# Kernel optimization log

Measured on AMD Instinct MI355X. Metric: run time of the kernel, lower is better.

## Reference

```python
import jax, jax.numpy as jnp
import numpy as np

N_DST = 25000
LEAKY = 0.2
EPS = 1e-5


def _params(dim_node=128, dim_edge=128, dim_time=100, dim_out=128):
    ks = jax.random.split(jax.random.key(1), 8)
    dq = dim_node + dim_time
    dk = dim_node + dim_edge + dim_time
    do = dim_node + dim_out
    p = {
        'w_t': jnp.asarray((1.0 / 10 ** np.linspace(0, 9, dim_time, dtype=np.float32)).reshape(dim_time, 1)),
        'b_t': jnp.zeros((dim_time,), jnp.float32),
        'Wq': jax.random.normal(ks[0], (dim_out, dq), jnp.float32) * (dq ** -0.5),
        'bq': jnp.zeros((dim_out,), jnp.float32),
        'Wk': jax.random.normal(ks[1], (dim_out, dk), jnp.float32) * (dk ** -0.5),
        'bk': jnp.zeros((dim_out,), jnp.float32),
        'Wv': jax.random.normal(ks[2], (dim_out, dk), jnp.float32) * (dk ** -0.5),
        'bv': jnp.zeros((dim_out,), jnp.float32),
        'Wout': jax.random.normal(ks[3], (dim_out, do), jnp.float32) * (do ** -0.5),
        'bout': jnp.zeros((dim_out,), jnp.float32),
        'ln_w': jnp.ones((dim_out,), jnp.float32),
        'ln_b': jnp.zeros((dim_out,), jnp.float32),
    }
    return p


def setup_inputs() -> dict:
    key = jax.random.key(0)
    k1, k2, k3, k4, k5 = jax.random.split(key, 5)
    E = 400000
    inp = {
        'h': jax.random.normal(k1, (425000, 128), jnp.float32),
        'f': jax.random.normal(k2, (E, 128), jnp.float32),
        'dt': jax.random.uniform(k3, (E,), jnp.float32) * 1e4,
        'src_idx': jax.random.randint(k4, (E,), 0, 425000, jnp.int32),
        'dst_idx': jax.random.randint(k5, (E,), 0, N_DST, jnp.int32),
    }
    inp.update(_params())
    return inp


def reference(h, f, dt, src_idx, dst_idx, w_t, b_t, Wq, bq, Wk, bk, Wv, bv, Wout, bout, ln_w, ln_b):
    num_head = 2
    dim_out = Wq.shape[0]
    E = dt.shape[0]
    # time encoding: cos(Linear(t))
    time_feat = jnp.cos(dt[:, None] * w_t[:, 0][None, :] + b_t)        # [E, dt]
    zero_time = jnp.cos(b_t)[None, :]                                   # [1, dt]
    zero_time_feat = jnp.broadcast_to(zero_time, (N_DST, b_t.shape[0]))
    # Q from dst nodes (first N_DST rows of h), gathered per edge
    q_nodes = jnp.concatenate([h[:N_DST], zero_time_feat], axis=1) @ Wq.T + bq  # [N_DST, dim_out]
    Q = q_nodes[dst_idx]                                                # [E, dim_out]
    kv_in = jnp.concatenate([h[src_idx], f, time_feat], axis=1)         # [E, dn+de+dt]
    K = kv_in @ Wk.T + bk
    V = kv_in @ Wv.T + bv
    dh = dim_out // num_head
    Qh = Q.reshape(E, num_head, dh)
    Kh = K.reshape(E, num_head, dh)
    Vh = V.reshape(E, num_head, dh)
    score = jax.nn.leaky_relu(jnp.sum(Qh * Kh, axis=2), LEAKY)          # [E, H]
    # edge softmax over incoming edges per dst node
    m = jax.ops.segment_max(score, dst_idx, num_segments=N_DST)         # [N_DST, H]
    e = jnp.exp(score - m[dst_idx])
    s = jax.ops.segment_sum(e, dst_idx, num_segments=N_DST)
    att = e / s[dst_idx]                                                # [E, H]
    Vw = (Vh * att[:, :, None]).reshape(E, dim_out)
    agg = jax.ops.segment_sum(Vw, dst_idx, num_segments=N_DST)          # [N_DST, dim_out]
    rst = jnp.concatenate([agg, h[:N_DST]], axis=1) @ Wout.T + bout
    rst = jax.nn.relu(rst)
    mu = jnp.mean(rst, axis=-1, keepdims=True)
    var = jnp.mean((rst - mu) ** 2, axis=-1, keepdims=True)
    return (rst - mu) * jax.lax.rsqrt(var + EPS) * ln_w + ln_b
```

## Files before the change

### kernel.cpp

```cpp
#include <hip/hip_runtime.h>
#include <math.h>

#define N_DST   25000
#define DN      128
#define DE      128
#define DTF     100
#define DKV     356
#define KP      384
#define DQ      228
#define DOUT    128
#define LEAKY   0.2f
#define LN_EPS  1e-5f
#define LDA     392

#define OFF_V       0ull
#define OFF_SCORE   102400000ull
#define OFF_QN      105600000ull
#define OFF_WS      118400000ull
#define OFF_WT      118700000ull
#define OFF_CNT     118900000ull
#define OFF_OFFS    119000000ull
#define OFF_CURSOR  119100004ull
#define OFF_RANK    119200004ull

typedef __attribute__((ext_vector_type(8))) short short8;
typedef __attribute__((ext_vector_type(4))) float f32x4;

__device__ __forceinline__ unsigned short f2bf(float x) {
    union { float f; unsigned u; } v; v.f = x;
    unsigned r = v.u + 0x7FFFu + ((v.u >> 16) & 1u);
    return (unsigned short)(r >> 16);
}
__device__ __forceinline__ float bf2f(unsigned short u) {
    union { unsigned u; float f; } v; v.u = ((unsigned)u) << 16;
    return v.f;
}

__global__ __launch_bounds__(128) void k_prepw(const float* __restrict__ Wk,
                                               const float* __restrict__ Wv,
                                               unsigned short* __restrict__ WS) {
    const int n = blockIdx.x;
    const float* src = (n < 128) ? &Wk[(size_t)n * DKV] : &Wv[(size_t)(n - 128) * DKV];
    const int c16 = n >> 4, t16 = n & 15;
    for (int k = threadIdx.x; k < KP; k += 128) {
        float v = (k < DKV) ? src[k] : 0.f;
        int kc = k >> 5, qd = (k >> 3) & 3, j = k & 7;
        WS[(size_t)(((kc * 16 + c16) * 64 + qd * 16 + t16) * 8 + j)] = f2bf(v);
    }
}

__global__ __launch_bounds__(128) void k_prepwt(const float* __restrict__ Wout,
                                                float* __restrict__ WT) {
    const int k = blockIdx.x;
    const int j = threadIdx.x;
    WT[k * 128 + j] = Wout[(size_t)j * 256 + k];
}

__global__ __launch_bounds__(128) void k_qnodes(const float* __restrict__ h,
                                                const float* __restrict__ Wq,
                                                const float* __restrict__ bq,
                                                const float* __restrict__ b_t,
                                                float* __restrict__ qn) {
    __shared__ float wq_s[128 * 132];
    __shared__ float hrow[8 * 128];
    const int j = threadIdx.x;

    for (int k4 = 0; k4 < 128; k4 += 4) {
        float4 w = *(const float4*)&Wq[j * DQ + k4];
        *(float4*)&wq_s[j * 132 + k4] = w;
    }
    float cq = bq[j];
    for (int k = 0; k < DTF; ++k)
        cq += Wq[j * DQ + 128 + k] * cosf(b_t[k]);
    __syncthreads();

    for (int r0 = blockIdx.x * 8; r0 < N_DST; r0 += gridDim.x * 8) {
        for (int u = j; u < 256; u += 128) {
            int rr = u >> 5, q = u & 31;
            int r = r0 + rr;
            float4 v = make_float4(0.f, 0.f, 0.f, 0.f);
            if (r < N_DST) v = *(const float4*)&h[(size_t)r * DN + q * 4];
            *(float4*)&hrow[rr * 128 + q * 4] = v;
        }
        __syncthreads();
        float acc[8];
        #pragma unroll
        for (int rr = 0; rr < 8; ++rr) acc[rr] = cq;
        for (int k4 = 0; k4 < 128; k4 += 4) {
            float4 wv = *(float4*)&wq_s[j * 132 + k4];
            #pragma unroll
            for (int rr = 0; rr < 8; ++rr) {
                float4 hv = *(float4*)&hrow[rr * 128 + k4];
                acc[rr] += hv.x * wv.x + hv.y * wv.y + hv.z * wv.z + hv.w * wv.w;
            }
        }
        #pragma unroll
        for (int rr = 0; rr < 8; ++rr)
            if (r0 + rr < N_DST) qn[(size_t)(r0 + rr) * DOUT + j] = acc[rr];
        __syncthreads();
    }
}

__global__ void k_hist(const int* __restrict__ dst, int* __restrict__ cnt, int E) {
    int i = blockIdx.x * 256 + threadIdx.x;
    if (i < E) atomicAdd(&cnt[dst[i]], 1);
}

__global__ __launch_bounds__(256) void k_scan(const int* __restrict__ cnt,
                                              int* __restrict__ offs,
                                              int* __restrict__ cursor) {
    __shared__ int totals[256];
    __shared__ int bases[257];
    const int t = threadIdx.x;
    const int STRIP = (N_DST + 255) / 256;
    int s = 0;
    for (int i = 0; i < STRIP; ++i) {
        int idx = t * STRIP + i;
        if (idx < N_DST) s += cnt[idx];
    }
    totals[t] = s;
    __syncthreads();
    if (t == 0) {
        int run = 0;
        for (int i = 0; i < 256; ++i) { bases[i] = run; run += totals[i]; }
        bases[256] = run;
    }
    __syncthreads();
    int run = bases[t];
    for (int i = 0; i < STRIP; ++i) {
        int idx = t * STRIP + i;
        if (idx < N_DST) {
            offs[idx] = run;
            cursor[idx] = run;
            run += cnt[idx];
        }
    }
    if (t == 0) offs[N_DST] = bases[256];
}

__global__ void k_scatter(const int* __restrict__ dst, int* __restrict__ cursor,
                          int* __restrict__ rank, int E) {
    int i = blockIdx.x * 256 + threadIdx.x;
    if (i < E) {
        int d = dst[i];
        int pos = atomicAdd(&cursor[d], 1);
        rank[i] = pos;
    }
}

__global__ __launch_bounds__(256, 3) void k_edge(const float* __restrict__ h,
                                                 const float* __restrict__ f,
                                                 const float* __restrict__ dtv,
                                                 const int* __restrict__ src_idx,
                                                 const int* __restrict__ dst_idx,
                                                 const int* __restrict__ rank,
                                                 const float* __restrict__ w_t,
                                                 const float* __restrict__ b_t,
                                                 const unsigned short* __restrict__ WS,
                                                 const float* __restrict__ bk,
                                                 const float* __restrict__ bv,
                                                 const float* __restrict__ qn,
                                                 unsigned short* __restrict__ Vout,
                                                 float* __restrict__ score,
                                                 int E) {
    __shared__ unsigned short At[64 * LDA];
    __shared__ int sidx[64];
    __shared__ int didx[64];
    __shared__ int rks[64];

    const int tid = threadIdx.x;
    const int e0  = blockIdx.x * 64;

    if (tid < 64) {
        int ge = min(e0 + tid, E - 1);
        sidx[tid] = src_idx[ge];
        didx[tid] = dst_idx[ge];
        rks[tid]  = rank[ge];
    }
    __syncthreads();

    {
        const int e  = tid >> 2;
        const int qb = tid & 3;
        const int ge = min(e0 + e, E - 1);
        const int s  = sidx[e];
        const float dte = dtv[ge];
        const float* hb = &h[(size_t)s * DN];
        const float* fb = &f[(size_t)ge * DE];
        float4 buf[8];

        #pragma unroll
        for (int it = 0; it < 8; ++it) buf[it] = *(const float4*)&hb[qb * 4 + it * 16];
        #pragma unroll
        for (int it = 0; it < 8; ++it) {
            int c = qb * 4 + it * 16;
            union { unsigned short us[4]; uint2 u2; } pk;
            pk.us[0] = f2bf(buf[it].x); pk.us[1] = f2bf(buf[it].y);
            pk.us[2] = f2bf(buf[it].z); pk.us[3] = f2bf(buf[it].w);
            *(uint2*)&At[e * LDA + c] = pk.u2;
        }
        #pragma unroll
        for (int it = 0; it < 8; ++it) buf[it] = *(const float4*)&fb[qb * 4 + it * 16];
        #pragma unroll
        for (int it = 0; it < 8; ++it) {
            int c = 128 + qb * 4 + it * 16;
            union { unsigned short us[4]; uint2 u2; } pk;
            pk.us[0] = f2bf(buf[it].x); pk.us[1] = f2bf(buf[it].y);
            pk.us[2] = f2bf(buf[it].z); pk.us[3] = f2bf(buf[it].w);
            *(uint2*)&At[e * LDA + c] = pk.u2;
        }
        #pragma unroll
        for (int it = 0; it < 8; ++it) {
            int t0 = qb * 4 + it * 16;
            float4 v = make_float4(0.f, 0.f, 0.f, 0.f);
            if (t0 < DTF) {
                v.x = cosf(dte * w_t[t0 + 0] + b_t[t0 + 0]);
                v.y = cosf(dte * w_t[t0 + 1] + b_t[t0 + 1]);
                v.z = cosf(dte * w_t[t0 + 2] + b_t[t0 + 2]);
                v.w = cosf(dte * w_t[t0 + 3] + b_t[t0 + 3]);
            }
            union { unsigned short us[4]; uint2 u2; } pk;
            pk.us[0] = f2bf(v.x); pk.us[1] = f2bf(v.y);
            pk.us[2] = f2bf(v.z); pk.us[3] = f2bf(v.w);
            *(uint2*)&At[e * LDA + 256 + t0] = pk.u2;
        }
    }
    __syncthreads();

    const int lane = tid & 63;
    const int w    = tid >> 6;
    const int t16  = lane & 15;
    const int qd   = lane >> 4;
    const int w4   = w * 4;

    f32x4 acc[4][4];
    #pragma unroll
    for (int r = 0; r < 4; ++r)
        #pragma unroll
        for (int c = 0; c < 4; ++c)
            acc[r][c] = (f32x4){0.f, 0.f, 0.f, 0.f};

    short8 aC[4], aN[4], bC[4], bN[4];
    #pragma unroll
    for (int r = 0; r < 4; ++r)
        aC[r] = *(const short8*)&At[(r * 16 + t16) * LDA + qd * 8];
    #pragma unroll
    for (int c = 0; c < 4; ++c)
        bC[c] = *(const short8*)(WS + (size_t)((0 * 16 + w4 + c) * 64 + lane) * 8);

    #pragma unroll 1
    for (int kc = 0; kc < 12; kc += 2) {
        #pragma unroll
        for (int r = 0; r < 4; ++r)
            aN[r] = *(const short8*)&At[(r * 16 + t16) * LDA + (kc + 1) * 32 + qd * 8];
        #pragma unroll
        for (int c = 0; c < 4; ++c)
            bN[c] = *(const short8*)(WS + (size_t)(((kc + 1) * 16 + w4 + c) * 64 + lane) * 8);
        #pragma unroll
        for (int r = 0; r < 4; ++r)
            #pragma unroll
            for (int c = 0; c < 4; ++c)
                acc[r][c] = __builtin_amdgcn_mfma_f32_16x16x32_bf16(aC[r], bC[c], acc[r][c], 0, 0, 0);
        if (kc + 2 < 12) {
            #pragma unroll
            for (int r = 0; r < 4; ++r)
                aC[r] = *(const short8*)&At[(r * 16 + t16) * LDA + (kc + 2) * 32 + qd * 8];
            #pragma unroll
            for (int c = 0; c < 4; ++c)
                bC[c] = *(const short8*)(WS + (size_t)(((kc + 2) * 16 + w4 + c) * 64 + lane) * 8);
        }
        #pragma unroll
        for (int r = 0; r < 4; ++r)
            #pragma unroll
            for (int c = 0; c < 4; ++c)
                acc[r][c] = __builtin_amdgcn_mfma_f32_16x16x32_bf16(aN[r], bN[c], acc[r][c], 0, 0, 0);
    }

    if (w >= 2) {
        const int vc0 = (w - 2) * 64;
        #pragma unroll
        for (int c = 0; c < 4; ++c) {
            const int vcol = vc0 + c * 16 + t16;
            const float bvv = bv[vcol];
            #pragma unroll
            for (int r = 0; r < 4; ++r) {
                #pragma unroll
                for (int i = 0; i < 4; ++i) {
                    int el = r * 16 + qd * 4 + i;
                    int ge = e0 + el;
                    if (ge < E)
                        Vout[(size_t)rks[el] * DOUT + vcol] = f2bf(acc[r][c][i] + bvv);
                }
            }
        }
    } else {
        float bkc[4];
        #pragma unroll
        for (int c = 0; c < 4; ++c)
            bkc[c] = bk[w * 64 + c * 16 + t16];
        #pragma unroll
        for (int r = 0; r < 4; ++r) {
            #pragma unroll
            for (int i = 0; i < 4; ++i) {
                const int el = r * 16 + qd * 4 + i;
                const int d  = didx[el];
                const float* qrow = &qn[(size_t)d * DOUT + w * 64 + t16];
                float p = (acc[r][0][i] + bkc[0]) * qrow[0]
                        + (acc[r][1][i] + bkc[1]) * qrow[16]
                        + (acc[r][2][i] + bkc[2]) * qrow[32]
                        + (acc[r][3][i] + bkc[3]) * qrow[48];
                p += __shfl_xor(p, 1);
                p += __shfl_xor(p, 2);
                p += __shfl_xor(p, 4);
                p += __shfl_xor(p, 8);
                if (t16 == 0) {
                    int ge = e0 + el;
                    if (ge < E) {
                        float sc = (p >= 0.f) ? p : LEAKY * p;
                        score[(size_t)rks[el] * 2 + w] = sc;
                    }
                }
            }
        }
    }
}

__global__ __launch_bounds__(512) void k_dst(const unsigned short* __restrict__ V,
                                             const float* __restrict__ score,
                                             const int* __restrict__ offs,
                                             const float* __restrict__ h,
                                             const float* __restrict__ WT,
                                             const float* __restrict__ bout,
                                             const float* __restrict__ ln_w,
                                             const float* __restrict__ ln_b,
                                             float* __restrict__ out) {
    const int tid = threadIdx.x;
    const int s   = tid >> 5;
    const int t32 = tid & 31;
    const int d   = blockIdx.x * 16 + s;
    const bool valid = d < N_DST;
    const int beg = valid ? offs[d] : 0;
    const int end = valid ? offs[d + 1] : 0;

    __shared__ float inc[16][256];
    __shared__ float wchunk[64 * 128];

    float m0 = -1e30f, m1 = -1e30f;
    for (int i = beg + t32; i < end; i += 32) {
        float2 sc = *(const float2*)&score[(size_t)i * 2];
        m0 = fmaxf(m0, sc.x);
        m1 = fmaxf(m1, sc.y);
    }
    #pragma unroll
    for (int o = 1; o < 32; o <<= 1) {
        m0 = fmaxf(m0, __shfl_xor(m0, o));
        m1 = fmaxf(m1, __shfl_xor(m1, o));
    }
    const int   hd = t32 >> 4;
    const float mh = hd ? m1 : m0;

    float a0 = 0.f, a1 = 0.f, a2 = 0.f, a3 = 0.f, l = 0.f;
    int i = beg;
    for (; i + 1 < end; i += 2) {
        float s0 = score[(size_t)i * 2 + hd];
        float s1 = score[(size_t)(i + 1) * 2 + hd];
        ushort4 v0 = *(const ushort4*)&V[(size_t)i * DOUT + t32 * 4];
        ushort4 v1 = *(const ushort4*)&V[(size_t)(i + 1) * DOUT + t32 * 4];
        float w0 = __expf(s0 - mh);
        float w1 = __expf(s1 - mh);
        l += w0 + w1;
        a0 += w0 * bf2f(v0.x) + w1 * bf2f(v1.x);
        a1 += w0 * bf2f(v0.y) + w1 * bf2f(v1.y);
        a2 += w0 * bf2f(v0.z) + w1 * bf2f(v1.z);
        a3 += w0 * bf2f(v0.w) + w1 * bf2f(v1.w);
    }
    if (i < end) {
        float s0 = score[(size_t)i * 2 + hd];
        ushort4 v0 = *(const ushort4*)&V[(size_t)i * DOUT + t32 * 4];
        float w0 = __expf(s0 - mh);
        l += w0;
        a0 += w0 * bf2f(v0.x);
        a1 += w0 * bf2f(v0.y);
        a2 += w0 * bf2f(v0.z);
        a3 += w0 * bf2f(v0.w);
    }
    float inv = (l > 0.f) ? (1.f / l) : 0.f;
    inc[s][t32 * 4 + 0] = a0 * inv;
    inc[s][t32 * 4 + 1] = a1 * inv;
    inc[s][t32 * 4 + 2] = a2 * inv;
    inc[s][t32 * 4 + 3] = a3 * inv;
    {
        float4 hh = make_float4(0.f, 0.f, 0.f, 0.f);
        if (valid) hh = *(const float4*)&h[(size_t)d * DN + t32 * 4];
        *(float4*)&inc[s][128 + t32 * 4] = hh;
    }

    float4 r4 = *(const float4*)&bout[t32 * 4];
    #pragma unroll 1
    for (int ch = 0; ch < 4; ++ch) {
        __syncthreads();
        for (int u = tid; u < 2048; u += 512)
            *(float4*)&wchunk[u * 4] = *(const float4*)&WT[(size_t)ch * 8192 + u * 4];
        __syncthreads();
        #pragma unroll 4
        for (int kk = 0; kk < 64; ++kk) {
            float ic = inc[s][ch * 64 + kk];
            float4 w4 = *(float4*)&wchunk[kk * 128 + t32 * 4];
            r4.x += w4.x * ic;
            r4.y += w4.y * ic;
            r4.z += w4.z * ic;
            r4.w += w4.w * ic;
        }
    }
    r4.x = fmaxf(r4.x, 0.f);
    r4.y = fmaxf(r4.y, 0.f);
    r4.z = fmaxf(r4.z, 0.f);
    r4.w = fmaxf(r4.w, 0.f);

    float s1 = r4.x + r4.y + r4.z + r4.w;
    float s2 = r4.x * r4.x + r4.y * r4.y + r4.z * r4.z + r4.w * r4.w;
    #pragma unroll
    for (int o = 1; o < 32; o <<= 1) {
        s1 += __shfl_xor(s1, o);
        s2 += __shfl_xor(s2, o);
    }
    float mu  = s1 * (1.f / 128.f);
    float var = s2 * (1.f / 128.f) - mu * mu;
    float rsd = rsqrtf(var + LN_EPS);
    if (valid) {
        float4 lw = *(const float4*)&ln_w[t32 * 4];
        float4 lb = *(const float4*)&ln_b[t32 * 4];
        float4 o4;
        o4.x = (r4.x - mu) * rsd * lw.x + lb.x;
        o4.y = (r4.y - mu) * rsd * lw.y + lb.y;
        o4.z = (r4.z - mu) * rsd * lw.z + lb.z;
        o4.w = (r4.w - mu) * rsd * lw.w + lb.w;
        *(float4*)&out[(size_t)d * DOUT + t32 * 4] = o4;
    }
}

extern "C" void kernel_launch(void* const* d_in, const int* in_sizes, int n_in,
                              void* d_out, int out_size, void* d_ws, size_t ws_size,
                              hipStream_t stream) {
    const float* h       = (const float*)d_in[0];
    const float* f       = (const float*)d_in[1];
    const float* dt      = (const float*)d_in[2];
    const int*   src_idx = (const int*)d_in[3];
    const int*   dst_idx = (const int*)d_in[4];
    const float* w_t     = (const float*)d_in[5];
    const float* b_t     = (const float*)d_in[6];
    const float* Wq      = (const float*)d_in[7];
    const float* bq      = (const float*)d_in[8];
    const float* Wk      = (const float*)d_in[9];
    const float* bk      = (const float*)d_in[10];
    const float* Wv      = (const float*)d_in[11];
    const float* bv      = (const float*)d_in[12];
    const float* Wout    = (const float*)d_in[13];
    const float* bout    = (const float*)d_in[14];
    const float* ln_w    = (const float*)d_in[15];
    const float* ln_b    = (const float*)d_in[16];
    float*       out     = (float*)d_out;

    const int E = in_sizes[2];

    char* ws = (char*)d_ws;
    unsigned short* V  = (unsigned short*)(ws + OFF_V);
    float* score       = (float*)(ws + OFF_SCORE);
    float* qn          = (float*)(ws + OFF_QN);
    unsigned short* WS = (unsigned short*)(ws + OFF_WS);
    float* WT          = (float*)(ws + OFF_WT);
    int*   cnt         = (int*)(ws + OFF_CNT);
    int*   offs        = (int*)(ws + OFF_OFFS);
    int*   cursor      = (int*)(ws + OFF_CURSOR);
    int*   rank        = (int*)(ws + OFF_RANK);

    hipMemsetAsync(cnt, 0, N_DST * sizeof(int), stream);

    k_prepw<<<256, 128, 0, stream>>>(Wk, Wv, WS);
    k_prepwt<<<256, 128, 0, stream>>>(Wout, WT);
    k_qnodes<<<512, 128, 0, stream>>>(h, Wq, bq, b_t, qn);
    k_hist<<<(E + 255) / 256, 256, 0, stream>>>(dst_idx, cnt, E);
    k_scan<<<1, 256, 0, stream>>>(cnt, offs, cursor);
    k_scatter<<<(E + 255) / 256, 256, 0, stream>>>(dst_idx, cursor, rank, E);
    k_edge<<<(E + 63) / 64, 256, 0, stream>>>(h, f, dt, src_idx, dst_idx, rank,
                                              w_t, b_t, WS, bk, bv, qn, V, score, E);
    k_dst<<<(N_DST + 15) / 16, 512, 0, stream>>>(V, score, offs, h, WT, bout,
                                                 ln_w, ln_b, out);
}
```

Measured before the change: 875.3 us.

## Write V/score in edge order, gather via CSR edge list; fast cos; rework qnodes

The edge kernel now writes V and score rows in original edge order, giving coalesced stores. k_scatter builds a CSR edge list, and the destination kernel gathers rows through that indirection instead of reading a pre-sorted layout. Time-encoding cos is replaced by a hardware cos with range reduction via fract. The Q-node projection now keeps weights in registers and splits K across two half-blocks, one block per 16 rows. Gathers in k_dst become random row reads, and the fast cos is less accurate for large arguments.

```diff
diff --git a/kernel.cpp b/kernel.cpp
--- a/kernel.cpp
+++ b/kernel.cpp
@@ -12,6 +12,7 @@
 #define LEAKY   0.2f
 #define LN_EPS  1e-5f
 #define LDA     392
+#define INV2PI  0.15915494309189535f
 
 #define OFF_V       0ull
 #define OFF_SCORE   102400000ull
@@ -21,7 +22,7 @@
 #define OFF_CNT     118900000ull
 #define OFF_OFFS    119000000ull
 #define OFF_CURSOR  119100004ull
-#define OFF_RANK    119200004ull
+#define OFF_ELIST   119200004ull
 
 typedef __attribute__((ext_vector_type(8))) short short8;
 typedef __attribute__((ext_vector_type(4))) float f32x4;
@@ -34,6 +35,9 @@
 __device__ __forceinline__ float bf2f(unsigned short u) {
     union { unsigned u; float f; } v; v.u = ((unsigned)u) << 16;
     return v.f;
+}
+__device__ __forceinline__ float fastcos(float x) {
+    return __builtin_amdgcn_cosf(__builtin_amdgcn_fractf(x * INV2PI));
 }
 
 __global__ __launch_bounds__(128) void k_prepw(const float* __restrict__ Wk,
@@ -56,48 +60,64 @@
     WT[k * 128 + j] = Wout[(size_t)j * 256 + k];
 }
 
-__global__ __launch_bounds__(128) void k_qnodes(const float* __restrict__ h,
+__global__ __launch_bounds__(256) void k_qnodes(const float* __restrict__ h,
                                                 const float* __restrict__ Wq,
                                                 const float* __restrict__ bq,
                                                 const float* __restrict__ b_t,
                                                 float* __restrict__ qn) {
-    __shared__ float wq_s[128 * 132];
-    __shared__ float hrow[8 * 128];
-    const int j = threadIdx.x;
-
-    for (int k4 = 0; k4 < 128; k4 += 4) {
-        float4 w = *(const float4*)&Wq[j * DQ + k4];
-        *(float4*)&wq_s[j * 132 + k4] = w;
-    }
-    float cq = bq[j];
-    for (int k = 0; k < DTF; ++k)
-        cq += Wq[j * DQ + 128 + k] * cosf(b_t[k]);
+    __shared__ float hrows[16 * 128];
+    __shared__ float part[16 * 128];
+    const int tid = threadIdx.x;
+    const int j  = tid & 127;
+    const int kh = tid >> 7;
+
+    float wq[64];
+    #pragma unroll
+    for (int k = 0; k < 64; k += 4) {
+        float4 w = *(const float4*)&Wq[j * DQ + kh * 64 + k];
+        wq[k] = w.x; wq[k + 1] = w.y; wq[k + 2] = w.z; wq[k + 3] = w.w;
+    }
+    float cq = 0.f;
+    if (kh == 0) {
+        cq = bq[j];
+        for (int k = 0; k < DTF; ++k)
+            cq += Wq[j * DQ + 128 + k] * fastcos(b_t[k]);
+    }
+
+    const int r0 = blockIdx.x * 16;
+    for (int u = tid; u < 512; u += 256) {
+        int rr = u >> 5, q = u & 31;
+        int r = r0 + rr;
+        float4 v = make_float4(0.f, 0.f, 0.f, 0.f);
+        if (r < N_DST) v = *(const float4*)&h[(size_t)r * DN + q * 4];
+        *(float4*)&hrows[rr * 128 + q * 4] = v;
+    }
     __syncthreads();
 
-    for (int r0 = blockIdx.x * 8; r0 < N_DST; r0 += gridDim.x * 8) {
-        for (int u = j; u < 256; u += 128) {
-            int rr = u >> 5, q = u & 31;
+    float acc[16];
+    #pragma unroll
+    for (int rr = 0; rr < 16; ++rr) acc[rr] = 0.f;
+    #pragma unroll
+    for (int k4 = 0; k4 < 64; k4 += 4) {
+        float w0 = wq[k4], w1 = wq[k4 + 1], w2 = wq[k4 + 2], w3 = wq[k4 + 3];
+        #pragma unroll
+        for (int rr = 0; rr < 16; ++rr) {
+            float4 hv = *(float4*)&hrows[rr * 128 + kh * 64 + k4];
+            acc[rr] += w0 * hv.x + w1 * hv.y + w2 * hv.z + w3 * hv.w;
+        }
+    }
+    if (kh == 1) {
+        #pragma unroll
+        for (int rr = 0; rr < 16; ++rr) part[rr * 128 + j] = acc[rr];
+    }
+    __syncthreads();
+    if (kh == 0) {
+        #pragma unroll
+        for (int rr = 0; rr < 16; ++rr) {
             int r = r0 + rr;
-            float4 v = make_float4(0.f, 0.f, 0.f, 0.f);
-            if (r < N_DST) v = *(const float4*)&h[(size_t)r * DN + q * 4];
-            *(float4*)&hrow[rr * 128 + q * 4] = v;
-        }
-        __syncthreads();
-        float acc[8];
-        #pragma unroll
-        for (int rr = 0; rr < 8; ++rr) acc[rr] = cq;
-        for (int k4 = 0; k4 < 128; k4 += 4) {
-            float4 wv = *(float4*)&wq_s[j * 132 + k4];
-            #pragma unroll
-            for (int rr = 0; rr < 8; ++rr) {
-                float4 hv = *(float4*)&hrow[rr * 128 + k4];
-                acc[rr] += hv.x * wv.x + hv.y * wv.y + hv.z * wv.z + hv.w * wv.w;
-            }
-        }
-        #pragma unroll
-        for (int rr = 0; rr < 8; ++rr)
-            if (r0 + rr < N_DST) qn[(size_t)(r0 + rr) * DOUT + j] = acc[rr];
-        __syncthreads();
+            if (r < N_DST)
+                qn[(size_t)r * DOUT + j] = acc[rr] + part[rr * 128 + j] + cq;
+        }
     }
 }
 
@@ -139,12 +159,12 @@
 }
 
 __global__ void k_scatter(const int* __restrict__ dst, int* __restrict__ cursor,
-                          int* __restrict__ rank, int E) {
+                          int* __restrict__ elist, int E) {
     int i = blockIdx.x * 256 + threadIdx.x;
     if (i < E) {
         int d = dst[i];
         int pos = atomicAdd(&cursor[d], 1);
-        rank[i] = pos;
+        elist[pos] = i;
     }
 }
 
@@ -153,7 +173,6 @@
                                                  const float* __restrict__ dtv,
                                                  const int* __restrict__ src_idx,
                                                  const int* __restrict__ dst_idx,
-                                                 const int* __restrict__ rank,
                                                  const float* __restrict__ w_t,
                                                  const float* __restrict__ b_t,
                                                  const unsigned short* __restrict__ WS,
@@ -166,7 +185,6 @@
     __shared__ unsigned short At[64 * LDA];
     __shared__ int sidx[64];
     __shared__ int didx[64];
-    __shared__ int rks[64];
 
     const int tid = threadIdx.x;
     const int e0  = blockIdx.x * 64;
@@ -175,7 +193,6 @@
         int ge = min(e0 + tid, E - 1);
         sidx[tid] = src_idx[ge];
         didx[tid] = dst_idx[ge];
-        rks[tid]  = rank[ge];
     }
     __syncthreads();
 
@@ -187,37 +204,29 @@
         const float dte = dtv[ge];
         const float* hb = &h[(size_t)s * DN];
         const float* fb = &f[(size_t)ge * DE];
-        float4 buf[8];
-
-        #pragma unroll
-        for (int it = 0; it < 8; ++it) buf[it] = *(const float4*)&hb[qb * 4 + it * 16];
-        #pragma unroll
-        for (int it = 0; it < 8; ++it) {
-            int c = qb * 4 + it * 16;
+        float4 buf[16];
+
+        #pragma unroll
+        for (int it = 0; it < 8; ++it) buf[it]     = *(const float4*)&hb[qb * 4 + it * 16];
+        #pragma unroll
+        for (int it = 0; it < 8; ++it) buf[8 + it] = *(const float4*)&fb[qb * 4 + it * 16];
+        #pragma unroll
+        for (int it = 0; it < 16; ++it) {
+            int c = (it < 8) ? (qb * 4 + it * 16) : (128 + qb * 4 + (it - 8) * 16);
             union { unsigned short us[4]; uint2 u2; } pk;
             pk.us[0] = f2bf(buf[it].x); pk.us[1] = f2bf(buf[it].y);
             pk.us[2] = f2bf(buf[it].z); pk.us[3] = f2bf(buf[it].w);
             *(uint2*)&At[e * LDA + c] = pk.u2;
         }
         #pragma unroll
-        for (int it = 0; it < 8; ++it) buf[it] = *(const float4*)&fb[qb * 4 + it * 16];
-        #pragma unroll
-        for (int it = 0; it < 8; ++it) {
-            int c = 128 + qb * 4 + it * 16;
-            union { unsigned short us[4]; uint2 u2; } pk;
-            pk.us[0] = f2bf(buf[it].x); pk.us[1] = f2bf(buf[it].y);
-            pk.us[2] = f2bf(buf[it].z); pk.us[3] = f2bf(buf[it].w);
-            *(uint2*)&At[e * LDA + c] = pk.u2;
-        }
-        #pragma unroll
         for (int it = 0; it < 8; ++it) {
             int t0 = qb * 4 + it * 16;
             float4 v = make_float4(0.f, 0.f, 0.f, 0.f);
             if (t0 < DTF) {
-                v.x = cosf(dte * w_t[t0 + 0] + b_t[t0 + 0]);
-                v.y = cosf(dte * w_t[t0 + 1] + b_t[t0 + 1]);
-                v.z = cosf(dte * w_t[t0 + 2] + b_t[t0 + 2]);
-                v.w = cosf(dte * w_t[t0 + 3] + b_t[t0 + 3]);
+                v.x = fastcos(dte * w_t[t0 + 0] + b_t[t0 + 0]);
+                v.y = fastcos(dte * w_t[t0 + 1] + b_t[t0 + 1]);
+                v.z = fastcos(dte * w_t[t0 + 2] + b_t[t0 + 2]);
+                v.w = fastcos(dte * w_t[t0 + 3] + b_t[t0 + 3]);
             }
             union { unsigned short us[4]; uint2 u2; } pk;
             pk.us[0] = f2bf(v.x); pk.us[1] = f2bf(v.y);
@@ -246,7 +255,7 @@
         aC[r] = *(const short8*)&At[(r * 16 + t16) * LDA + qd * 8];
     #pragma unroll
     for (int c = 0; c < 4; ++c)
-        bC[c] = *(const short8*)(WS + (size_t)((0 * 16 + w4 + c) * 64 + lane) * 8);
+        bC[c] = *(const short8*)(WS + (size_t)((w4 + c) * 64 + lane) * 8);
 
     #pragma unroll 1
     for (int kc = 0; kc < 12; kc += 2) {
@@ -278,18 +287,20 @@
 
     if (w >= 2) {
         const int vc0 = (w - 2) * 64;
-        #pragma unroll
-        for (int c = 0; c < 4; ++c) {
-            const int vcol = vc0 + c * 16 + t16;
-            const float bvv = bv[vcol];
+        float bvv[4];
+        #pragma unroll
+        for (int c = 0; c < 4; ++c) bvv[c] = bv[vc0 + c * 16 + t16];
+        #pragma unroll
+        for (int r = 0; r < 4; ++r) {
             #pragma unroll
-            for (int r = 0; r < 4; ++r) {
-                #pragma unroll
-                for (int i = 0; i < 4; ++i) {
-                    int el = r * 16 + qd * 4 + i;
-                    int ge = e0 + el;
-                    if (ge < E)
-                        Vout[(size_t)rks[el] * DOUT + vcol] = f2bf(acc[r][c][i] + bvv);
+            for (int i = 0; i < 4; ++i) {
+                int el = r * 16 + qd * 4 + i;
+                int ge = e0 + el;
+                if (ge < E) {
+                    unsigned short* vr = &Vout[(size_t)ge * DOUT + vc0 + t16];
+                    #pragma unroll
+                    for (int c = 0; c < 4; ++c)
+                        vr[c * 16] = f2bf(acc[r][c][i] + bvv[c]);
                 }
             }
         }
@@ -317,7 +328,7 @@
                     int ge = e0 + el;
                     if (ge < E) {
                         float sc = (p >= 0.f) ? p : LEAKY * p;
-                        score[(size_t)rks[el] * 2 + w] = sc;
+                        score[(size_t)ge * 2 + w] = sc;
                     }
                 }
             }
@@ -328,6 +339,7 @@
 __global__ __launch_bounds__(512) void k_dst(const unsigned short* __restrict__ V,
                                              const float* __restrict__ score,
                                              const int* __restrict__ offs,
+                                             const int* __restrict__ elist,
                                              const float* __restrict__ h,
                                              const float* __restrict__ WT,
                                              const float* __restrict__ bout,
@@ -347,7 +359,8 @@
 
     float m0 = -1e30f, m1 = -1e30f;
     for (int i = beg + t32; i < end; i += 32) {
-        float2 sc = *(const float2*)&score[(size_t)i * 2];
+        int e = elist[i];
+        float2 sc = *(const float2*)&score[(size_t)e * 2];
         m0 = fmaxf(m0, sc.x);
         m1 = fmaxf(m1, sc.y);
     }
@@ -362,10 +375,11 @@
     float a0 = 0.f, a1 = 0.f, a2 = 0.f, a3 = 0.f, l = 0.f;
     int i = beg;
     for (; i + 1 < end; i += 2) {
-        float s0 = score[(size_t)i * 2 + hd];
-        float s1 = score[(size_t)(i + 1) * 2 + hd];
-        ushort4 v0 = *(const ushort4*)&V[(size_t)i * DOUT + t32 * 4];
-        ushort4 v1 = *(const ushort4*)&V[(size_t)(i + 1) * DOUT + t32 * 4];
+        int ea = elist[i], eb = elist[i + 1];
+        float s0 = score[(size_t)ea * 2 + hd];
+        float s1 = score[(size_t)eb * 2 + hd];
+        ushort4 v0 = *(const ushort4*)&V[(size_t)ea * DOUT + t32 * 4];
+        ushort4 v1 = *(const ushort4*)&V[(size_t)eb * DOUT + t32 * 4];
         float w0 = __expf(s0 - mh);
         float w1 = __expf(s1 - mh);
         l += w0 + w1;
@@ -375,8 +389,9 @@
         a3 += w0 * bf2f(v0.w) + w1 * bf2f(v1.w);
     }
     if (i < end) {
-        float s0 = score[(size_t)i * 2 + hd];
-        ushort4 v0 = *(const ushort4*)&V[(size_t)i * DOUT + t32 * 4];
+        int ea = elist[i];
+        float s0 = score[(size_t)ea * 2 + hd];
+        ushort4 v0 = *(const ushort4*)&V[(size_t)ea * DOUT + t32 * 4];
         float w0 = __expf(s0 - mh);
         l += w0;
         a0 += w0 * bf2f(v0.x);
@@ -472,18 +487,18 @@
     int*   cnt         = (int*)(ws + OFF_CNT);
     int*   offs        = (int*)(ws + OFF_OFFS);
     int*   cursor      = (int*)(ws + OFF_CURSOR);
-    int*   rank        = (int*)(ws + OFF_RANK);
+    int*   elist       = (int*)(ws + OFF_ELIST);
 
     hipMemsetAsync(cnt, 0, N_DST * sizeof(int), stream);
 
     k_prepw<<<256, 128, 0, stream>>>(Wk, Wv, WS);
     k_prepwt<<<256, 128, 0, stream>>>(Wout, WT);
-    k_qnodes<<<512, 128, 0, stream>>>(h, Wq, bq, b_t, qn);
+    k_qnodes<<<(N_DST + 15) / 16, 256, 0, stream>>>(h, Wq, bq, b_t, qn);
     k_hist<<<(E + 255) / 256, 256, 0, stream>>>(dst_idx, cnt, E);
     k_scan<<<1, 256, 0, stream>>>(cnt, offs, cursor);
-    k_scatter<<<(E + 255) / 256, 256, 0, stream>>>(dst_idx, cursor, rank, E);
-    k_edge<<<(E + 63) / 64, 256, 0, stream>>>(h, f, dt, src_idx, dst_idx, rank,
+    k_scatter<<<(E + 255) / 256, 256, 0, stream>>>(dst_idx, cursor, elist, E);
+    k_edge<<<(E + 63) / 64, 256, 0, stream>>>(h, f, dt, src_idx, dst_idx,
                                               w_t, b_t, WS, bk, bv, qn, V, score, E);
-    k_dst<<<(N_DST + 15) / 16, 512, 0, stream>>>(V, score, offs, h, WT, bout,
+    k_dst<<<(N_DST + 15) / 16, 512, 0, stream>>>(V, score, offs, elist, h, WT, bout,
                                                  ln_w, ln_b, out);
 }
```

Result: faster. 799.0 us (-8.7%).
